# Kernel optimization log

Measured on AMD Instinct MI355X. Metric: run time of the kernel, lower is better.

The kernel has to match this reference:

```python
import jax, jax.numpy as jnp
import numpy as np

B, H, W = 8, 384, 384
KH = KW = 3
STRIDE, PAD = 1, 1


def setup_inputs() -> dict:
    key = jax.random.key(0)
    ks = jax.random.split(key, 5)
    pf = jax.random.normal(ks[0], (B, 3, H, W), jnp.float32)
    cf = jax.random.normal(ks[1], (B, 3, H, W), jnp.float32)
    mv = jax.random.normal(ks[2], (B, 2, H, W), jnp.float32)
    offset_w = jax.random.normal(ks[3], (18, 8, KH, KW), jnp.float32) * 0.05
    offset_b = jnp.zeros((18,), jnp.float32)
    deform_w = jax.random.normal(ks[4], (3, 3, KH, KW), jnp.float32) * 0.1
    return dict(pf=pf, cf=cf, mv=mv, offset_w=offset_w, offset_b=offset_b, deform_w=deform_w)


def _conv2d(x, w, b):
    y = jax.lax.conv_general_dilated(
        x, w, window_strides=(STRIDE, STRIDE),
        padding=((PAD, PAD), (PAD, PAD)),
        dimension_numbers=('NCHW', 'OIHW', 'NCHW'))
    return y + b[None, :, None, None]


def _deform_conv2d(x, offset, w):
    # x: [B, Cin, H, W]; offset: [B, 2*KH*KW, Ho, Wo] (torchvision order: per tap k -> (dy, dx))
    Bn, Cin, Hn, Wn = x.shape
    Ho, Wo = offset.shape[2], offset.shape[3]
    K = KH * KW
    off = offset.reshape(Bn, K, 2, Ho, Wo)
    ky = jnp.repeat(jnp.arange(KH), KW).astype(x.dtype)   # [K] kernel row offset
    kx = jnp.tile(jnp.arange(KW), KH).astype(x.dtype)     # [K] kernel col offset
    base_y = (jnp.arange(Ho) * STRIDE - PAD).astype(x.dtype)
    base_x = (jnp.arange(Wo) * STRIDE - PAD).astype(x.dtype)
    # sampling positions p = p0 + p_k + delta_p_k, shape [B, K, Ho, Wo]
    py = off[:, :, 0] + ky[None, :, None, None] + base_y[None, None, :, None]
    px = off[:, :, 1] + kx[None, :, None, None] + base_x[None, None, None, :]
    y0 = jnp.floor(py)
    x0 = jnp.floor(px)
    wy = py - y0  # bilinear weights, [B, K, Ho, Wo]
    wx = px - x0

    def gather(yi, xi):
        # zero padding outside the image (torchvision semantics)
        valid = (yi >= 0) & (yi < Hn) & (xi >= 0) & (xi < Wn)
        yc = jnp.clip(yi, 0, Hn - 1).astype(jnp.int32)
        xc = jnp.clip(xi, 0, Wn - 1).astype(jnp.int32)
        v = jax.vmap(lambda im, y, xg: im[:, y, xg])(x, yc, xc)  # [B, Cin, K, Ho, Wo]
        return v * valid[:, None].astype(x.dtype)

    v00 = gather(y0, x0)
    v01 = gather(y0, x0 + 1)
    v10 = gather(y0 + 1, x0)
    v11 = gather(y0 + 1, x0 + 1)
    wy_ = wy[:, None]  # broadcast over channel dim
    wx_ = wx[:, None]
    samp = (v00 * (1 - wy_) * (1 - wx_) + v01 * (1 - wy_) * wx_
            + v10 * wy_ * (1 - wx_) + v11 * wy_ * wx_)  # [B, Cin, K, Ho, Wo]
    # weighted accumulation over taps and input channels (no bias)
    return jnp.einsum('oik,bikhw->bohw', w.reshape(w.shape[0], w.shape[1], K), samp)


def reference(pf, cf, mv, offset_w, offset_b, deform_w):
    x = jnp.concatenate([pf, cf, mv], axis=1)          # [B, 8, H, W]
    offset = _conv2d(x, offset_w, offset_b)            # [B, 18, H, W]
    return _deform_conv2d(pf, offset, deform_w)        # [B, 3, H, W]
```

## Files before the change

kernel.cpp:

```cpp
#include <hip/hip_runtime.h>


#define Bn 8
#define Hn 384
#define Wn 384
#define HWn (Hn * Wn)
#define TILE 16
#define PH 8
#define PT 32
#define TRS 216
#define TCS 12

#define OFF_PTILE 0
#define SZ_PTILE (PT * PT * 4)
#define OFF_T8   SZ_PTILE
#define SZ_T8U   4864
#define SMEM_FLOATS (OFF_T8 + SZ_T8U)

typedef float f32x4 __attribute__((ext_vector_type(4)));
typedef short s16x8 __attribute__((ext_vector_type(8)));

__device__ inline unsigned pack_bf16(float lo, float hi) {
    return (__float_as_uint(hi) & 0xffff0000u) | (__float_as_uint(lo) >> 16);
}
__device__ inline unsigned short rne_bf16(float f) {
    unsigned u = __float_as_uint(f);
    u += 0x7fffu + ((u >> 16) & 1u);
    return (unsigned short)(u >> 16);
}

__global__ void prep_bw(const float* __restrict__ ow, unsigned short* __restrict__ bwg) {
    const int idx = blockIdx.x * 64 + threadIdx.x;
    const int sg   = idx >> 6;
    const int lane = idx & 63;
    const int s  = sg >> 1;
    const int nt = sg & 1;
    const int am = lane & 15;
    const int g  = lane >> 4;
    const int oc = nt * 16 + am;
    const int t  = 4 * s + g;
    union { unsigned short h[8]; s16x8 v; } F;
#pragma unroll
    for (int c = 0; c < 8; ++c) {
        float w = 0.f;
        if (t < 9 && oc < 18) w = ow[oc * 72 + c * 9 + t];
        F.h[c] = rne_bf16(w);
    }
    ((s16x8*)bwg)[idx] = F.v;
}

__global__ __launch_bounds__(256, 4) void guided_cnn_fused(
    const float* __restrict__ pf, const float* __restrict__ cf,
    const float* __restrict__ mv, const s16x8* __restrict__ bwg,
    const float* __restrict__ ob, const float* __restrict__ dw,
    float* __restrict__ out)
{
    __shared__ float smem[SMEM_FLOATS];

    const int tid = threadIdx.x;
    const int b = blockIdx.z;
    const int tileY0 = blockIdx.y * TILE;
    const int tileX0 = blockIdx.x * TILE;
    const int oy = tileY0 - PH;
    const int ox = tileX0 - PH;

    float* ptile4 = smem + OFF_PTILE;
    float* t8i    = smem + OFF_T8;

    const int lane = tid & 63;
    const int wv   = tid >> 6;
    const int am   = lane & 15;
    const int g    = lane >> 4;

    s16x8 bfrag[3][2];
#pragma unroll
    for (int s = 0; s < 3; ++s)
#pragma unroll
        for (int nt = 0; nt < 2; ++nt)
            bfrag[s][nt] = bwg[(s * 2 + nt) * 64 + lane];

    for (int p = tid; p < PT * PT; p += 256) {
        const int row = p >> 5;
        const int col = p & 31;
        const int gy = oy + row, gx = ox + col;
        const bool v = ((unsigned)gy < (unsigned)Hn) && ((unsigned)gx < (unsigned)Wn);
        const size_t gidx = (size_t)b * 3 * HWn + gy * Wn + gx;
        f32x4 q;
        q[0] = v ? pf[gidx] : 0.f;
        q[1] = v ? pf[gidx + HWn] : 0.f;
        q[2] = v ? pf[gidx + 2 * HWn] : 0.f;
        q[3] = 0.f;
        *(f32x4*)(ptile4 + p * 4) = q;
    }
    for (int i = tid; i < 8 * 324; i += 256) {
        const int c   = i / 324;
        const int rem = i - c * 324;
        const int row = rem / 18;
        const int col = rem - row * 18;
        const int gy = tileY0 + row - 1, gx = tileX0 + col - 1;
        const float* plane;
        if (c < 3)      plane = pf + ((size_t)b * 3 + c) * HWn;
        else if (c < 6) plane = cf + ((size_t)b * 3 + (c - 3)) * HWn;
        else            plane = mv + ((size_t)b * 2 + (c - 6)) * HWn;
        const bool v = ((unsigned)gy < (unsigned)Hn) && ((unsigned)gx < (unsigned)Wn);
        t8i[row * TRS + col * TCS + c] = v ? plane[gy * Wn + gx] : 0.f;
    }
    __syncthreads();

    f32x4 acc[4][2];
#pragma unroll
    for (int mt = 0; mt < 4; ++mt)
#pragma unroll
        for (int nt = 0; nt < 2; ++nt)
            acc[mt][nt] = (f32x4){0.f, 0.f, 0.f, 0.f};

    const int t_of_g[3] = {0 + g, 4 + g, 8 + g};
#pragma unroll
    for (int mt = 0; mt < 4; ++mt) {
        const int mrow = wv * 4 + mt;
#pragma unroll
        for (int s = 0; s < 3; ++s) {
            const int t  = t_of_g[s];
            const bool tv = (t < 9);
            const int tc = tv ? t : 0;
            const int dy = tc / 3, dx = tc - dy * 3;
            const float* base = t8i + (mrow + dy) * TRS + (am + dx) * TCS;
            const f32x4 lo = *(const f32x4*)base;
            const f32x4 hi = *(const f32x4*)(base + 4);
            union { unsigned u[4]; s16x8 v; } A;
            A.u[0] = tv ? pack_bf16(lo[0], lo[1]) : 0u;
            A.u[1] = tv ? pack_bf16(lo[2], lo[3]) : 0u;
            A.u[2] = tv ? pack_bf16(hi[0], hi[1]) : 0u;
            A.u[3] = tv ? pack_bf16(hi[2], hi[3]) : 0u;
            acc[mt][0] = __builtin_amdgcn_mfma_f32_16x16x32_bf16(A.v, bfrag[s][0], acc[mt][0], 0, 0, 0);
            acc[mt][1] = __builtin_amdgcn_mfma_f32_16x16x32_bf16(A.v, bfrag[s][1], acc[mt][1], 0, 0, 0);
        }
    }
    __syncthreads();

    float* offb = smem + OFF_T8;
#pragma unroll
    for (int mt = 0; mt < 4; ++mt) {
        const int prow = wv * 4 + mt;
#pragma unroll
        for (int r = 0; r < 4; ++r) {
            const int pix = prow * 16 + (g * 4 + r);
            offb[pix * 19 + am] = acc[mt][0][r];
            if (am < 2) offb[pix * 19 + 16 + am] = acc[mt][1][r];
        }
    }
    __syncthreads();

    const int tx = tid & 15;
    const int ty = tid >> 4;
    const int x = tileX0 + tx;
    const int y = tileY0 + ty;

    float offs[18];
#pragma unroll
    for (int j = 0; j < 18; ++j) offs[j] = offb[tid * 19 + j] + ob[j];

    const float* p0 = pf + (size_t)b * 3 * HWn;
    float acc2[3] = {0.f, 0.f, 0.f};

#pragma unroll
    for (int k = 0; k < 9; ++k) {
        const int ky = k / 3;
        const int kx = k - ky * 3;
        const float py = offs[2 * k]     + (float)(y + ky - 1);
        const float px = offs[2 * k + 1] + (float)(x + kx - 1);
        const float y0f = floorf(py);
        const float x0f = floorf(px);
        const float wy = py - y0f;
        const float wx = px - x0f;
        const int y0 = (int)y0f, x0 = (int)x0f;
        const int y1 = y0 + 1,  x1 = x0 + 1;
        const bool vy0 = ((unsigned)y0 < (unsigned)Hn);
        const bool vy1 = ((unsigned)y1 < (unsigned)Hn);
        const bool vx0 = ((unsigned)x0 < (unsigned)Wn);
        const bool vx1 = ((unsigned)x1 < (unsigned)Wn);
        const int y0c = min(max(y0, 0), Hn - 1);
        const int y1c = min(max(y1, 0), Hn - 1);
        const int x0c = min(max(x0, 0), Wn - 1);
        const int x1c = min(max(x1, 0), Wn - 1);
        const float w00 = (1.f - wy) * (1.f - wx);
        const float w01 = (1.f - wy) * wx;
        const float w10 = wy * (1.f - wx);
        const float w11 = wy * wx;

        const int ty0 = y0c - oy, tx0 = x0c - ox;
        const int ty1 = y1c - oy, tx1 = x1c - ox;
        const bool inT = ((unsigned)ty0 < (unsigned)PT) && ((unsigned)ty1 < (unsigned)PT) &&
                         ((unsigned)tx0 < (unsigned)PT) && ((unsigned)tx1 < (unsigned)PT);

        if (inT) {
            const float m00 = (vy0 && vx0) ? w00 : 0.f;
            const float m01 = (vy0 && vx1) ? w01 : 0.f;
            const float m10 = (vy1 && vx0) ? w10 : 0.f;
            const float m11 = (vy1 && vx1) ? w11 : 0.f;
            const f32x4 q00 = *(const f32x4*)(ptile4 + (ty0 * PT + tx0) * 4);
            const f32x4 q01 = *(const f32x4*)(ptile4 + (ty0 * PT + tx1) * 4);
            const f32x4 q10 = *(const f32x4*)(ptile4 + (ty1 * PT + tx0) * 4);
            const f32x4 q11 = *(const f32x4*)(ptile4 + (ty1 * PT + tx1) * 4);
#pragma unroll
            for (int i = 0; i < 3; ++i) {
                const float s = m00 * q00[i] + m01 * q01[i] + m10 * q10[i] + m11 * q11[i];
#pragma unroll
                for (int o = 0; o < 3; ++o)
                    acc2[o] = fmaf(dw[o * 27 + i * 9 + k], s, acc2[o]);
            }
        } else {
            const int i00 = y0c * Wn + x0c;
            const int i01 = y0c * Wn + x1c;
            const int i10 = y1c * Wn + x0c;
            const int i11 = y1c * Wn + x1c;
#pragma unroll
            for (int i = 0; i < 3; ++i) {
                const float* pl = p0 + (size_t)i * HWn;
                const float v00 = (vy0 && vx0) ? pl[i00] : 0.f;
                const float v01 = (vy0 && vx1) ? pl[i01] : 0.f;
                const float v10 = (vy1 && vx0) ? pl[i10] : 0.f;
                const float v11 = (vy1 && vx1) ? pl[i11] : 0.f;
                const float s = w00 * v00 + w01 * v01 + w10 * v10 + w11 * v11;
#pragma unroll
                for (int o = 0; o < 3; ++o)
                    acc2[o] = fmaf(dw[o * 27 + i * 9 + k], s, acc2[o]);
            }
        }
    }

#pragma unroll
    for (int o = 0; o < 3; ++o) {
        out[(((size_t)b * 3 + o) * Hn + y) * Wn + x] = acc2[o];
    }
}

extern "C" void kernel_launch(void* const* d_in, const int* in_sizes, int n_in,
                              void* d_out, int out_size, void* d_ws, size_t ws_size,
                              hipStream_t stream) {
    const float* pf = (const float*)d_in[0];
    const float* cf = (const float*)d_in[1];
    const float* mv = (const float*)d_in[2];
    const float* ow = (const float*)d_in[3];
    const float* ob = (const float*)d_in[4];
    const float* dw = (const float*)d_in[5];
    float* out = (float*)d_out;
    unsigned short* bwg = (unsigned short*)d_ws;

    prep_bw<<<6, 64, 0, stream>>>(ow, bwg);
    dim3 grid(Wn / TILE, Hn / TILE, Bn);
    guided_cnn_fused<<<grid, 256, 0, stream>>>(pf, cf, mv, (const s16x8*)bwg, ob, dw, out);
}
```

Before: 137.7 us.

## Pre-pack conv input as bf16 in LDS, shrink halo tile, simplify deform sampling

```diff
diff --git a/kernel.cpp b/kernel.cpp
--- a/kernel.cpp
+++ b/kernel.cpp
@@ -6,10 +6,8 @@
 #define Wn 384
 #define HWn (Hn * Wn)
 #define TILE 16
-#define PH 8
-#define PT 32
-#define TRS 216
-#define TCS 12
+#define PH 6
+#define PT 28
 
 #define OFF_PTILE 0
 #define SZ_PTILE (PT * PT * 4)
@@ -20,9 +18,6 @@
 typedef float f32x4 __attribute__((ext_vector_type(4)));
 typedef short s16x8 __attribute__((ext_vector_type(8)));
 
-__device__ inline unsigned pack_bf16(float lo, float hi) {
-    return (__float_as_uint(hi) & 0xffff0000u) | (__float_as_uint(lo) >> 16);
-}
 __device__ inline unsigned short rne_bf16(float f) {
     unsigned u = __float_as_uint(f);
     u += 0x7fffu + ((u >> 16) & 1u);
@@ -49,7 +44,7 @@
     ((s16x8*)bwg)[idx] = F.v;
 }
 
-__global__ __launch_bounds__(256, 4) void guided_cnn_fused(
+__global__ __launch_bounds__(256, 5) void guided_cnn_fused(
     const float* __restrict__ pf, const float* __restrict__ cf,
     const float* __restrict__ mv, const s16x8* __restrict__ bwg,
     const float* __restrict__ ob, const float* __restrict__ dw,
@@ -65,7 +60,7 @@
     const int ox = tileX0 - PH;
 
     float* ptile4 = smem + OFF_PTILE;
-    float* t8i    = smem + OFF_T8;
+    float* t8b    = smem + OFF_T8;
 
     const int lane = tid & 63;
     const int wv   = tid >> 6;
@@ -80,8 +75,8 @@
             bfrag[s][nt] = bwg[(s * 2 + nt) * 64 + lane];
 
     for (int p = tid; p < PT * PT; p += 256) {
-        const int row = p >> 5;
-        const int col = p & 31;
+        const int row = p / PT;
+        const int col = p - row * PT;
         const int gy = oy + row, gx = ox + col;
         const bool v = ((unsigned)gy < (unsigned)Hn) && ((unsigned)gx < (unsigned)Wn);
         const size_t gidx = (size_t)b * 3 * HWn + gy * Wn + gx;
@@ -92,18 +87,27 @@
         q[3] = 0.f;
         *(f32x4*)(ptile4 + p * 4) = q;
     }
-    for (int i = tid; i < 8 * 324; i += 256) {
-        const int c   = i / 324;
-        const int rem = i - c * 324;
-        const int row = rem / 18;
-        const int col = rem - row * 18;
+    for (int p = tid; p < 324; p += 256) {
+        const int row = p / 18;
+        const int col = p - row * 18;
         const int gy = tileY0 + row - 1, gx = tileX0 + col - 1;
-        const float* plane;
-        if (c < 3)      plane = pf + ((size_t)b * 3 + c) * HWn;
-        else if (c < 6) plane = cf + ((size_t)b * 3 + (c - 3)) * HWn;
-        else            plane = mv + ((size_t)b * 2 + (c - 6)) * HWn;
         const bool v = ((unsigned)gy < (unsigned)Hn) && ((unsigned)gx < (unsigned)Wn);
-        t8i[row * TRS + col * TCS + c] = v ? plane[gy * Wn + gx] : 0.f;
+        const size_t base = (size_t)b * 3 * HWn + gy * Wn + gx;
+        float c0 = v ? pf[base] : 0.f;
+        float c1 = v ? pf[base + HWn] : 0.f;
+        float c2 = v ? pf[base + 2 * HWn] : 0.f;
+        float c3 = v ? cf[base] : 0.f;
+        float c4 = v ? cf[base + HWn] : 0.f;
+        float c5 = v ? cf[base + 2 * HWn] : 0.f;
+        const size_t mbase = (size_t)b * 2 * HWn + gy * Wn + gx;
+        float c6 = v ? mv[mbase] : 0.f;
+        float c7 = v ? mv[mbase + HWn] : 0.f;
+        union { unsigned u[4]; f32x4 f; } P;
+        P.u[0] = (unsigned)rne_bf16(c0) | ((unsigned)rne_bf16(c1) << 16);
+        P.u[1] = (unsigned)rne_bf16(c2) | ((unsigned)rne_bf16(c3) << 16);
+        P.u[2] = (unsigned)rne_bf16(c4) | ((unsigned)rne_bf16(c5) << 16);
+        P.u[3] = (unsigned)rne_bf16(c6) | ((unsigned)rne_bf16(c7) << 16);
+        *(f32x4*)(t8b + p * 4) = P.f;
     }
     __syncthreads();
 
@@ -114,24 +118,16 @@
         for (int nt = 0; nt < 2; ++nt)
             acc[mt][nt] = (f32x4){0.f, 0.f, 0.f, 0.f};
 
-    const int t_of_g[3] = {0 + g, 4 + g, 8 + g};
 #pragma unroll
     for (int mt = 0; mt < 4; ++mt) {
         const int mrow = wv * 4 + mt;
 #pragma unroll
         for (int s = 0; s < 3; ++s) {
-            const int t  = t_of_g[s];
-            const bool tv = (t < 9);
-            const int tc = tv ? t : 0;
+            const int tap = 4 * s + g;
+            const int tc  = tap < 9 ? tap : 8;
             const int dy = tc / 3, dx = tc - dy * 3;
-            const float* base = t8i + (mrow + dy) * TRS + (am + dx) * TCS;
-            const f32x4 lo = *(const f32x4*)base;
-            const f32x4 hi = *(const f32x4*)(base + 4);
-            union { unsigned u[4]; s16x8 v; } A;
-            A.u[0] = tv ? pack_bf16(lo[0], lo[1]) : 0u;
-            A.u[1] = tv ? pack_bf16(lo[2], lo[3]) : 0u;
-            A.u[2] = tv ? pack_bf16(hi[0], hi[1]) : 0u;
-            A.u[3] = tv ? pack_bf16(hi[2], hi[3]) : 0u;
+            union { f32x4 f; s16x8 v; } A;
+            A.f = *(const f32x4*)(t8b + ((mrow + dy) * 18 + (am + dx)) * 4);
             acc[mt][0] = __builtin_amdgcn_mfma_f32_16x16x32_bf16(A.v, bfrag[s][0], acc[mt][0], 0, 0, 0);
             acc[mt][1] = __builtin_amdgcn_mfma_f32_16x16x32_bf16(A.v, bfrag[s][1], acc[mt][1], 0, 0, 0);
         }
@@ -167,49 +163,45 @@
     for (int k = 0; k < 9; ++k) {
         const int ky = k / 3;
         const int kx = k - ky * 3;
-        const float py = offs[2 * k]     + (float)(y + ky - 1);
-        const float px = offs[2 * k + 1] + (float)(x + kx - 1);
-        const float y0f = floorf(py);
-        const float x0f = floorf(px);
-        const float wy = py - y0f;
-        const float wx = px - x0f;
-        const int y0 = (int)y0f, x0 = (int)x0f;
-        const int y1 = y0 + 1,  x1 = x0 + 1;
-        const bool vy0 = ((unsigned)y0 < (unsigned)Hn);
-        const bool vy1 = ((unsigned)y1 < (unsigned)Hn);
-        const bool vx0 = ((unsigned)x0 < (unsigned)Wn);
-        const bool vx1 = ((unsigned)x1 < (unsigned)Wn);
-        const int y0c = min(max(y0, 0), Hn - 1);
-        const int y1c = min(max(y1, 0), Hn - 1);
-        const int x0c = min(max(x0, 0), Wn - 1);
-        const int x1c = min(max(x1, 0), Wn - 1);
+        const float rpy = offs[2 * k]     + (float)(ty + ky - 1 + PH);
+        const float rpx = offs[2 * k + 1] + (float)(tx + kx - 1 + PH);
+        const float y0f = floorf(rpy);
+        const float x0f = floorf(rpx);
+        const float wy = rpy - y0f;
+        const float wx = rpx - x0f;
+        const int ty0 = (int)y0f;
+        const int tx0 = (int)x0f;
         const float w00 = (1.f - wy) * (1.f - wx);
         const float w01 = (1.f - wy) * wx;
         const float w10 = wy * (1.f - wx);
         const float w11 = wy * wx;
 
-        const int ty0 = y0c - oy, tx0 = x0c - ox;
-        const int ty1 = y1c - oy, tx1 = x1c - ox;
-        const bool inT = ((unsigned)ty0 < (unsigned)PT) && ((unsigned)ty1 < (unsigned)PT) &&
-                         ((unsigned)tx0 < (unsigned)PT) && ((unsigned)tx1 < (unsigned)PT);
-
+        const bool inT = ((unsigned)ty0 < (unsigned)(PT - 1)) &&
+                         ((unsigned)tx0 < (unsigned)(PT - 1));
         if (inT) {
-            const float m00 = (vy0 && vx0) ? w00 : 0.f;
-            const float m01 = (vy0 && vx1) ? w01 : 0.f;
-            const float m10 = (vy1 && vx0) ? w10 : 0.f;
-            const float m11 = (vy1 && vx1) ? w11 : 0.f;
-            const f32x4 q00 = *(const f32x4*)(ptile4 + (ty0 * PT + tx0) * 4);
-            const f32x4 q01 = *(const f32x4*)(ptile4 + (ty0 * PT + tx1) * 4);
-            const f32x4 q10 = *(const f32x4*)(ptile4 + (ty1 * PT + tx0) * 4);
-            const f32x4 q11 = *(const f32x4*)(ptile4 + (ty1 * PT + tx1) * 4);
+            const float* base = ptile4 + (ty0 * PT + tx0) * 4;
+            const f32x4 q00 = *(const f32x4*)(base);
+            const f32x4 q01 = *(const f32x4*)(base + 4);
+            const f32x4 q10 = *(const f32x4*)(base + 4 * PT);
+            const f32x4 q11 = *(const f32x4*)(base + 4 * PT + 4);
 #pragma unroll
             for (int i = 0; i < 3; ++i) {
-                const float s = m00 * q00[i] + m01 * q01[i] + m10 * q10[i] + m11 * q11[i];
+                const float s = w00 * q00[i] + w01 * q01[i] + w10 * q10[i] + w11 * q11[i];
 #pragma unroll
                 for (int o = 0; o < 3; ++o)
                     acc2[o] = fmaf(dw[o * 27 + i * 9 + k], s, acc2[o]);
             }
         } else {
+            const int y0 = ty0 + oy, x0 = tx0 + ox;
+            const int y1 = y0 + 1,  x1 = x0 + 1;
+            const bool vy0 = ((unsigned)y0 < (unsigned)Hn);
+            const bool vy1 = ((unsigned)y1 < (unsigned)Hn);
+            const bool vx0 = ((unsigned)x0 < (unsigned)Wn);
+            const bool vx1 = ((unsigned)x1 < (unsigned)Wn);
+            const int y0c = min(max(y0, 0), Hn - 1);
+            const int y1c = min(max(y1, 0), Hn - 1);
+            const int x0c = min(max(x0, 0), Wn - 1);
+            const int x1c = min(max(x1, 0), Wn - 1);
             const int i00 = y0c * Wn + x0c;
             const int i01 = y0c * Wn + x1c;
             const int i10 = y1c * Wn + x0c;
```

New measurement: 118.6 us. 1.16x faster.
